# Optimization experiments

Measured on AMD Instinct MI355X. Metric: run time of the kernel, lower is better.

Reference implementation:

```python
import jax, jax.numpy as jnp
import numpy as np

EPS = 1e-12

def setup_inputs() -> dict:
    key = jax.random.key(0)
    k1, k2 = jax.random.split(key)
    N, L, C = 32768, 256, 64
    mu = jax.random.uniform(k1, (N, L), dtype=jnp.float32)
    leaf_scores = jax.random.normal(k2, (L, C), dtype=jnp.float32)
    return {"mu": mu, "leaf_scores": leaf_scores}

def reference(mu, leaf_scores):
    # log path probabilities, clamped for numerical safety: (N, L)
    log_mu = jnp.log(jnp.clip(mu, EPS, None))
    # per-leaf class log-probs: (L, C)
    logQ = jax.nn.log_softmax(leaf_scores, axis=1)
    # y[n,k] = logsumexp_l( log_mu[n,l] + logQ[l,k] )  -> (N, C)
    scores = log_mu[:, :, None] + logQ[None, :, :]  # (N, L, C)
    return jax.scipy.special.logsumexp(scores, axis=1)
```

## Files before the change

kernel.cpp:

```cpp
#include <hip/hip_runtime.h>
#include <math.h>

#define NN 32768
#define LL 256
#define CC 64

typedef __attribute__((ext_vector_type(8))) _Float16 half8;
typedef __attribute__((ext_vector_type(4))) float f32x4;

__global__ __launch_bounds__(256) void fused_leaf_mix_kernel(
    const float* __restrict__ mu, const float* __restrict__ scores,
    float* __restrict__ out) {
    __shared__ float Bs[8192];

    const int tid  = threadIdx.x;
    const int wid  = tid >> 6;
    const int lane = tid & 63;
    const int quad = lane >> 4;
    const int m    = lane & 15;

    float vn[8];
    {
        const int g = wid * 8;
        const int s = g >> 2, q = g & 3;
        const float* srow = scores + (s * 32 + q * 8) * CC + lane;
        #pragma unroll
        for (int j = 0; j < 8; ++j) vn[j] = srow[j * CC];
    }

    const size_t row = (size_t)blockIdx.x * 64 + wid * 16 + m;
    const float* arow = mu + row * LL + quad * 8;
    float4 a[16];
    #pragma unroll
    for (int s = 0; s < 8; ++s) {
        a[2 * s]     = *(const float4*)(arow + s * 32);
        a[2 * s + 1] = *(const float4*)(arow + s * 32 + 4);
    }

    #pragma unroll
    for (int gi = 0; gi < 8; ++gi) {
        const int g = wid * 8 + gi;
        const int s = g >> 2, q = g & 3;
        float v[8];
        #pragma unroll
        for (int j = 0; j < 8; ++j) v[j] = vn[j];
        if (gi < 7) {
            const int gn = g + 1;
            const int sn = gn >> 2, qn = gn & 3;
            const float* srow = scores + (sn * 32 + qn * 8) * CC + lane;
            #pragma unroll
            for (int j = 0; j < 8; ++j) vn[j] = srow[j * CC];
        }
        half8 h;
        #pragma unroll
        for (int j = 0; j < 8; ++j) {
            float mx = v[j];
            #pragma unroll
            for (int off = 32; off > 0; off >>= 1)
                mx = fmaxf(mx, __shfl_xor(mx, off));
            const float e = __expf(v[j] - mx);
            float sum = e;
            #pragma unroll
            for (int off = 32; off > 0; off >>= 1)
                sum += __shfl_xor(sum, off);
            h[j] = (_Float16)__fdividef(e, sum);
        }
        ((half8*)Bs)[(s * 4 + quad) * 64 + q * 16 + m] = h;
    }
    __syncthreads();

    f32x4 acc[4] = {{0.f, 0.f, 0.f, 0.f}, {0.f, 0.f, 0.f, 0.f},
                    {0.f, 0.f, 0.f, 0.f}, {0.f, 0.f, 0.f, 0.f}};

    #pragma unroll
    for (int s = 0; s < 8; ++s) {
        half8 ah;
        ah[0] = (_Float16)a[2 * s].x;     ah[1] = (_Float16)a[2 * s].y;
        ah[2] = (_Float16)a[2 * s].z;     ah[3] = (_Float16)a[2 * s].w;
        ah[4] = (_Float16)a[2 * s + 1].x; ah[5] = (_Float16)a[2 * s + 1].y;
        ah[6] = (_Float16)a[2 * s + 1].z; ah[7] = (_Float16)a[2 * s + 1].w;
        #pragma unroll
        for (int tt = 0; tt < 4; ++tt) {
            const half8 b = ((const half8*)Bs)[(s * 4 + tt) * 64 + lane];
            acc[tt] = __builtin_amdgcn_mfma_f32_16x16x32_f16(ah, b, acc[tt], 0, 0, 0);
        }
    }

    const size_t outRow0 = (size_t)blockIdx.x * 64 + wid * 16 + quad * 4;
    #pragma unroll
    for (int tt = 0; tt < 4; ++tt)
        #pragma unroll
        for (int r = 0; r < 4; ++r)
            out[(outRow0 + r) * CC + tt * 16 + m] = __logf(acc[tt][r]);
}

extern "C" void kernel_launch(void* const* d_in, const int* in_sizes, int n_in,
                              void* d_out, int out_size, void* d_ws, size_t ws_size,
                              hipStream_t stream) {
    const float* mu     = (const float*)d_in[0];
    const float* scores = (const float*)d_in[1];
    float* out = (float*)d_out;
    (void)d_ws; (void)ws_size;

    fused_leaf_mix_kernel<<<NN / 64, 256, 0, stream>>>(mu, scores, out);
}
```

Measured before the change: 90.96 us.

## Compute leaf softmax per-thread with row loads and XOR-swizzled LDS stores

Each thread now loads one full leaf row of 64 scores with vector loads and computes max, exp and sum locally. This replaces the previous wave-wide shuffle reductions done per element. The normalized halves are written to LDS as scalar 2-byte stores into an XOR-swizzled layout, and the MFMA B-fragment reads use the matching swizzle to avoid bank conflicts. This removes many cross-lane shuffles, but it adds 64 scattered half-word LDS stores per thread and more register pressure from holding 64 floats.

```diff
diff --git a/kernel.cpp b/kernel.cpp
--- a/kernel.cpp
+++ b/kernel.cpp
@@ -19,69 +19,66 @@
     const int quad = lane >> 4;
     const int m    = lane & 15;
 
-    float vn[8];
+    f32x4 sv[16];
     {
-        const int g = wid * 8;
-        const int s = g >> 2, q = g & 3;
-        const float* srow = scores + (s * 32 + q * 8) * CC + lane;
+        const f32x4* srow = (const f32x4*)(scores + tid * CC);
         #pragma unroll
-        for (int j = 0; j < 8; ++j) vn[j] = srow[j * CC];
+        for (int c = 0; c < 16; ++c) sv[c] = srow[c];
     }
 
     const size_t row = (size_t)blockIdx.x * 64 + wid * 16 + m;
     const float* arow = mu + row * LL + quad * 8;
-    float4 a[16];
+    f32x4 a[16];
     #pragma unroll
     for (int s = 0; s < 8; ++s) {
-        a[2 * s]     = *(const float4*)(arow + s * 32);
-        a[2 * s + 1] = *(const float4*)(arow + s * 32 + 4);
+        a[2 * s]     = *(const f32x4*)(arow + s * 32);
+        a[2 * s + 1] = *(const f32x4*)(arow + s * 32 + 4);
     }
 
+    float mx = fmaxf(fmaxf(sv[0][0], sv[0][1]), fmaxf(sv[0][2], sv[0][3]));
     #pragma unroll
-    for (int gi = 0; gi < 8; ++gi) {
-        const int g = wid * 8 + gi;
-        const int s = g >> 2, q = g & 3;
-        float v[8];
+    for (int c = 1; c < 16; ++c)
+        mx = fmaxf(mx, fmaxf(fmaxf(sv[c][0], sv[c][1]),
+                             fmaxf(sv[c][2], sv[c][3])));
+    float sum = 0.f;
+    #pragma unroll
+    for (int c = 0; c < 16; ++c) {
+        sv[c][0] = __expf(sv[c][0] - mx);
+        sv[c][1] = __expf(sv[c][1] - mx);
+        sv[c][2] = __expf(sv[c][2] - mx);
+        sv[c][3] = __expf(sv[c][3] - mx);
+        sum += (sv[c][0] + sv[c][1]) + (sv[c][2] + sv[c][3]);
+    }
+    const float rs = __fdividef(1.0f, sum);
+
+    {
+        char* bs = (char*)Bs;
+        const int s = tid >> 5, q = (tid >> 3) & 3, j = tid & 7;
+        const int base = s * 4096 + q * 256 + j * 2;
+        const int qx = q << 4;
         #pragma unroll
-        for (int j = 0; j < 8; ++j) v[j] = vn[j];
-        if (gi < 7) {
-            const int gn = g + 1;
-            const int sn = gn >> 2, qn = gn & 3;
-            const float* srow = scores + (sn * 32 + qn * 8) * CC + lane;
-            #pragma unroll
-            for (int j = 0; j < 8; ++j) vn[j] = srow[j * CC];
+        for (int k = 0; k < 64; ++k) {
+            const _Float16 h = (_Float16)(sv[k >> 2][k & 3] * rs);
+            *(_Float16*)(bs + base + (k >> 4) * 1024 + (((k & 15) * 16) ^ qx)) = h;
         }
-        half8 h;
-        #pragma unroll
-        for (int j = 0; j < 8; ++j) {
-            float mx = v[j];
-            #pragma unroll
-            for (int off = 32; off > 0; off >>= 1)
-                mx = fmaxf(mx, __shfl_xor(mx, off));
-            const float e = __expf(v[j] - mx);
-            float sum = e;
-            #pragma unroll
-            for (int off = 32; off > 0; off >>= 1)
-                sum += __shfl_xor(sum, off);
-            h[j] = (_Float16)__fdividef(e, sum);
-        }
-        ((half8*)Bs)[(s * 4 + quad) * 64 + q * 16 + m] = h;
     }
     __syncthreads();
 
     f32x4 acc[4] = {{0.f, 0.f, 0.f, 0.f}, {0.f, 0.f, 0.f, 0.f},
                     {0.f, 0.f, 0.f, 0.f}, {0.f, 0.f, 0.f, 0.f}};
 
+    const char* bsr = (const char*)Bs;
+    const int rlane = (lane * 16) ^ (quad << 4);
     #pragma unroll
     for (int s = 0; s < 8; ++s) {
         half8 ah;
-        ah[0] = (_Float16)a[2 * s].x;     ah[1] = (_Float16)a[2 * s].y;
-        ah[2] = (_Float16)a[2 * s].z;     ah[3] = (_Float16)a[2 * s].w;
-        ah[4] = (_Float16)a[2 * s + 1].x; ah[5] = (_Float16)a[2 * s + 1].y;
-        ah[6] = (_Float16)a[2 * s + 1].z; ah[7] = (_Float16)a[2 * s + 1].w;
+        ah[0] = (_Float16)a[2 * s][0];     ah[1] = (_Float16)a[2 * s][1];
+        ah[2] = (_Float16)a[2 * s][2];     ah[3] = (_Float16)a[2 * s][3];
+        ah[4] = (_Float16)a[2 * s + 1][0]; ah[5] = (_Float16)a[2 * s + 1][1];
+        ah[6] = (_Float16)a[2 * s + 1][2]; ah[7] = (_Float16)a[2 * s + 1][3];
         #pragma unroll
         for (int tt = 0; tt < 4; ++tt) {
-            const half8 b = ((const half8*)Bs)[(s * 4 + tt) * 64 + lane];
+            const half8 b = *(const half8*)(bsr + (s * 4 + tt) * 1024 + rlane);
             acc[tt] = __builtin_amdgcn_mfma_f32_16x16x32_f16(ah, b, acc[tt], 0, 0, 0);
         }
     }
```

Result: faster. 79.74 us (-12.3%).
